# Performance work log

Measured on AMD Instinct MI355X. Metric: run time of the kernel, lower is better.

## Reference

```python
import jax, jax.numpy as jnp
import numpy as np

B, N, D = 8, 65536, 3
K = 64                 # num_centers
NPOINT = 4096
M = NPOINT // K * 2    # max_neighbors = 128
S = NPOINT // K        # fps samples per group = 64
NITER = 10             # KMeans default Niter


def _sqdist(src, dst):
    # ||s||^2 + ||d||^2 - 2 s.d   (same math as (s-d)^2 sum, GEMM form)
    s2 = (src ** 2).sum(-1)[:, :, None]          # [B,N,1]
    d2 = (dst ** 2).sum(-1)[:, None, :]          # [B,1,K]
    return s2 + d2 - 2.0 * jnp.einsum('bnd,bkd->bnk', src, dst)


def _kmeans(x):
    Bb, Nn, Dd = x.shape
    c = x[:, :K, :]
    bidx = jnp.arange(Bb)[:, None]               # broadcast with cl [B,N]
    for _ in range(NITER):
        cl = jnp.argmin(_sqdist(x, c), axis=2)   # [B,N] cluster codes
        c = jnp.zeros((Bb, K, Dd), x.dtype).at[bidx, cl].add(x)
        ncl = jnp.zeros((Bb, K), x.dtype).at[bidx, cl].add(1.0)
        c = c / ncl[:, :, None]
    return c


def _query_neighbor(x, centers):
    dist = _sqdist(x, centers)                   # [B,N,K]
    negd = -jnp.transpose(dist, (0, 2, 1))       # [B,K,N]
    _, nidx = jax.lax.top_k(negd, M)             # M nearest points per center
    bidx = jnp.arange(x.shape[0])[:, None, None]
    return x[bidx, nidx]                         # [B,K,M,3]


def _batch_fps(xyz, farthest0):
    # xyz: [B,G,Nn,3]; sequential farthest-point sampling per group
    Bb, G, Nn, _ = xyz.shape
    dist0 = jnp.full((Bb, G, Nn), 1e10, xyz.dtype)

    def step(carry, _):
        distance, farthest = carry
        centroid = jnp.take_along_axis(xyz, farthest[:, :, None, None], axis=2)  # [B,G,1,3]
        d = ((xyz - centroid) ** 2).sum(-1)       # [B,G,Nn]
        distance = jnp.minimum(distance, d)
        new_far = jnp.argmax(distance, -1).astype(farthest.dtype)
        return (distance, new_far), farthest      # store index BEFORE update

    _, idx = jax.lax.scan(step, (dist0, farthest0), None, length=S)
    idx = jnp.transpose(idx, (1, 2, 0))           # [B,G,S]
    idx3 = jnp.broadcast_to(idx[..., None], idx.shape + (3,))
    new_xyz = jnp.take_along_axis(xyz, idx3, axis=2)  # [B,G,S,3]
    return new_xyz.reshape(Bb, G * S, 3)


def setup_inputs() -> dict:
    key = jax.random.key(0)
    k1, k2 = jax.random.split(key)
    x = jax.random.normal(k1, (B, N, D), dtype=jnp.float32)
    farthest0 = jax.random.randint(k2, (B, K), 0, M, dtype=jnp.int32)
    return {"x": x, "farthest0": farthest0}


def reference(x, farthest0):
    centers = _kmeans(x)                  # [B,K,3]
    neighbor = _query_neighbor(x, centers)  # [B,K,M,3]
    new_xyz = _batch_fps(neighbor, farthest0)  # [B, NPOINT, 3]
    return new_xyz, centers
```

## Files before the change

kernel.cpp:

```cpp
#include <hip/hip_runtime.h>
#include <stdint.h>

#pragma clang fp contract(off)

#define B 8
#define N 65536
#define KC 64
#define M 128
#define S 64
#define NITER 10
#define NWAVES 16
#define HPAD 257
#define SAMPLE 8192
#define SCAP 2048
#define CAPG 3072
#define TCAP 4096
#define CSTRIDE 32
#define UPD_T 1024
#define RANGE 16384
#define NRANGE (N / RANGE)
#define PPT (RANGE / UPD_T)
#define GBATCH 2048

using u32 = unsigned int;
using u64 = unsigned long long;

__device__ __forceinline__ float sq3(float a, float b, float c) {
  return __fadd_rn(__fadd_rn(__fmul_rn(a, a), __fmul_rn(b, b)), __fmul_rn(c, c));
}
__device__ __forceinline__ float dot3(float x0, float x1, float x2,
                                      float c0, float c1, float c2) {
  return __fadd_rn(__fadd_rn(__fmul_rn(x0, c0), __fmul_rn(x1, c1)), __fmul_rn(x2, c2));
}
__device__ __forceinline__ float distf(float s2, float d2, float dt) {
  return __fsub_rn(__fadd_rn(s2, d2), __fmul_rn(2.0f, dt));
}
__device__ __forceinline__ u32 fkey(float f) {
  u32 u = __float_as_uint(f);
  return (u & 0x80000000u) ? ~u : (u | 0x80000000u);
}


__global__ void k_init_centers(const float* __restrict__ x, float* __restrict__ centers) {
  int i = blockIdx.x * blockDim.x + threadIdx.x;
  if (i >= B * KC * 3) return;
  int b = i / (KC * 3);
  int r = i % (KC * 3);
  centers[i] = x[(size_t)b * N * 3 + r];
}

__global__ void k_assign(const float* __restrict__ x, const float* __restrict__ centers,
                         unsigned char* __restrict__ cl) {
  __shared__ float4 cs[KC];
  int g = blockIdx.x;
  int b = g & 7;
  int chunk = g >> 3;
  int t = threadIdx.x;
  if (t < KC) {
    float a0 = centers[(b * KC + t) * 3 + 0];
    float a1 = centers[(b * KC + t) * 3 + 1];
    float a2 = centers[(b * KC + t) * 3 + 2];
    cs[t] = make_float4(a0, a1, a2, sq3(a0, a1, a2));
  }
  __syncthreads();
  int pr = chunk * 256 + t;
  const float2* xb2 = (const float2*)(x + (size_t)b * N * 3);
  float2 A = xb2[3 * pr], Bv = xb2[3 * pr + 1], C = xb2[3 * pr + 2];
  float s20 = sq3(A.x, A.y, Bv.x);
  float s21 = sq3(Bv.y, C.x, C.y);
  float best0 = __int_as_float(0x7f800000), best1 = best0;
  int bi0 = 0, bi1 = 0;
  for (int k = 0; k < KC; ++k) {
    float4 cc = cs[k];
    float d0 = distf(s20, cc.w, dot3(A.x, A.y, Bv.x, cc.x, cc.y, cc.z));
    float d1 = distf(s21, cc.w, dot3(Bv.y, C.x, C.y, cc.x, cc.y, cc.z));
    if (d0 < best0) { best0 = d0; bi0 = k; }
    if (d1 < best1) { best1 = d1; bi1 = k; }
  }
  *(unsigned short*)(cl + (size_t)b * N + 2 * pr) =
      (unsigned short)(bi0 | (bi1 << 8));
}

__global__ __launch_bounds__(UPD_T)
void k_cluster_update(const float* __restrict__ x, const unsigned char* __restrict__ cl,
                      float* __restrict__ centers) {
  __shared__ unsigned short midx[RANGE];
  __shared__ float bcoord[3][GBATCH + 1];
  __shared__ int woff[NWAVES];
  __shared__ int sCnt;
  int g = blockIdx.x;
  int bk = ((g & 7) << 6) | (g >> 3);
  int b = bk >> 6, k = bk & 63;
  int t = threadIdx.x, lane = t & 63, wid = t >> 6;
  const unsigned char* clb = cl + (size_t)b * N;
  const float* xb = x + (size_t)b * N * 3;
  float acc = 0.f;
  int cntAll = 0;

  for (int r = 0; r < NRANGE; ++r) {
    const uint4* cp = (const uint4*)(clb + r * RANGE);
    uint4 v = cp[t];
    u32 wsv[4] = {v.x, v.y, v.z, v.w};
    int m = 0;
#pragma unroll
    for (int j = 0; j < PPT; ++j)
      m += (((wsv[j >> 2] >> ((j & 3) * 8)) & 255u) == (u32)k);
    int incl = m;
#pragma unroll
    for (int o = 1; o < 64; o <<= 1) {
      int u = __shfl_up(incl, o);
      if (lane >= o) incl += u;
    }
    if (lane == 63) woff[wid] = incl;
    __syncthreads();
    if (t == 0) {
      int run = 0;
      for (int w = 0; w < NWAVES; ++w) { int vv = woff[w]; woff[w] = run; run += vv; }
      sCnt = run;
    }
    __syncthreads();
    int off = woff[wid] + incl - m;
    int mcnt = sCnt;
    int base = t * PPT;
#pragma unroll
    for (int j = 0; j < PPT; ++j) {
      if (((wsv[j >> 2] >> ((j & 3) * 8)) & 255u) == (u32)k)
        midx[off++] = (unsigned short)(base + j);
    }
    __syncthreads();
    for (int bo = 0; bo < mcnt; bo += GBATCH) {
      int bn = min(GBATCH, mcnt - bo);
      for (int i = t; i < bn; i += UPD_T) {
        int li = midx[bo + i];
        size_t src = ((size_t)(r * RANGE + li)) * 3;
        bcoord[0][i] = xb[src];
        bcoord[1][i] = xb[src + 1];
        bcoord[2][i] = xb[src + 2];
      }
      __syncthreads();
      if (wid == 0 && lane < 3) {
        const float* mb = &bcoord[lane][0];
        for (int i = 0; i < bn; ++i) acc = __fadd_rn(acc, mb[i]);
      }
      __syncthreads();
    }
    cntAll += mcnt;
    __syncthreads();
  }
  if (wid == 0 && lane < 3)
    centers[bk * 3 + lane] = __fdiv_rn(acc, (float)cntAll);
}

__global__ __launch_bounds__(256)
void k_thresh(const float* __restrict__ x, const float* __restrict__ centers,
              u32* __restrict__ thr, u32* __restrict__ cnt) {
  __shared__ u32 whist[4 * HPAD];
  __shared__ int sv[256];
  __shared__ u32 skeys[SCAP];
  __shared__ float4 scen;
  __shared__ u32 sSel;
  __shared__ int sNeed, sCntBin, sNum;
  int g = blockIdx.x;
  int bk = ((g & 7) << 6) | (g >> 3);
  int b = bk >> 6;
  int t = threadIdx.x, wid = t >> 6;
  if (t == 0) {
    float c0 = centers[bk * 3], c1 = centers[bk * 3 + 1], c2 = centers[bk * 3 + 2];
    scen = make_float4(c0, c1, c2, sq3(c0, c1, c2));
    cnt[bk * CSTRIDE] = 0;
    sNum = 0;
  }
  for (int i = t; i < 4 * HPAD; i += 256) whist[i] = 0;
  __syncthreads();
  float c0 = scen.x, c1 = scen.y, c2 = scen.z, d2 = scen.w;
  const float2* xb2 = (const float2*)(x + (size_t)b * N * 3);

  for (int p = t; p < SAMPLE / 2; p += 256) {
    float2 A = xb2[3 * p], Bv = xb2[3 * p + 1], C = xb2[3 * p + 2];
    float d0 = distf(sq3(A.x, A.y, Bv.x), d2, dot3(A.x, A.y, Bv.x, c0, c1, c2));
    float d1 = distf(sq3(Bv.y, C.x, C.y), d2, dot3(Bv.y, C.x, C.y, c0, c1, c2));
    atomicAdd(&whist[wid * HPAD + (fkey(d0) >> 24)], 1u);
    atomicAdd(&whist[wid * HPAD + (fkey(d1) >> 24)], 1u);
  }
  __syncthreads();
  int own = (int)(whist[0 * HPAD + t] + whist[1 * HPAD + t] +
                  whist[2 * HPAD + t] + whist[3 * HPAD + t]);
  sv[t] = own;
  __syncthreads();
  for (int off = 1; off < 256; off <<= 1) {
    int add = (t >= off) ? sv[t - off] : 0;
    __syncthreads();
    sv[t] += add;
    __syncthreads();
  }
  if (sv[t] >= M && sv[t] - own < M) {
    sSel = (u32)t; sNeed = M - (sv[t] - own); sCntBin = own;
  }
  __syncthreads();
  u32 selByte = sSel;
  int need = sNeed;
  int cntBin = sCntBin;
  u32 prefix = selByte << 24;

  if (cntBin <= SCAP) {
    for (int p = t; p < SAMPLE / 2; p += 256) {
      float2 A = xb2[3 * p], Bv = xb2[3 * p + 1], C = xb2[3 * p + 2];
      float d0 = distf(sq3(A.x, A.y, Bv.x), d2, dot3(A.x, A.y, Bv.x, c0, c1, c2));
      float d1 = distf(sq3(Bv.y, C.x, C.y), d2, dot3(Bv.y, C.x, C.y, c0, c1, c2));
      u32 k0 = fkey(d0), k1 = fkey(d1);
      if ((k0 >> 24) == selByte) skeys[atomicAdd(&sNum, 1)] = k0;
      if ((k1 >> 24) == selByte) skeys[atomicAdd(&sNum, 1)] = k1;
    }
    __syncthreads();
    int ne = sNum;
    for (int sh = 16; sh >= 0; sh -= 8) {
      whist[t] = 0;
      __syncthreads();
      for (int i = t; i < ne; i += 256) {
        u32 kk = skeys[i];
        if ((kk >> (sh + 8)) == (prefix >> (sh + 8)))
          atomicAdd(&whist[(kk >> sh) & 255u], 1u);
      }
      __syncthreads();
      int own2 = (int)whist[t];
      sv[t] = own2;
      __syncthreads();
      for (int off = 1; off < 256; off <<= 1) {
        int add = (t >= off) ? sv[t - off] : 0;
        __syncthreads();
        sv[t] += add;
        __syncthreads();
      }
      if (sv[t] >= need && sv[t] - own2 < need) {
        sSel = prefix | ((u32)t << sh);
        sNeed = need - (sv[t] - own2);
      }
      __syncthreads();
      prefix = sSel; need = sNeed;
      __syncthreads();
    }
    if (t == 0) thr[bk] = prefix;
  } else {
    if (t == 0) thr[bk] = prefix | 0x00FFFFFFu;
  }
}

__global__ __launch_bounds__(256)
void k_scatter_test(const float* __restrict__ x, const float* __restrict__ centers,
                    const u32* __restrict__ thr, u32* __restrict__ cnt,
                    u32* __restrict__ cand) {
  __shared__ float4 cs[KC];
  __shared__ u32 lthr[KC];
  __shared__ u64 wm0[4][KC], wm1[4][KC];
  __shared__ u32 wbase[4][KC];
  int g = blockIdx.x;
  int b = g & 7;
  int chunk = g >> 3;
  int t = threadIdx.x, lane = t & 63, wid = t >> 6;
  if (t < KC) {
    float a0 = centers[(b * KC + t) * 3 + 0];
    float a1 = centers[(b * KC + t) * 3 + 1];
    float a2 = centers[(b * KC + t) * 3 + 2];
    cs[t] = make_float4(a0, a1, a2, sq3(a0, a1, a2));
    lthr[t] = thr[b * KC + t];
  }
  __syncthreads();
  int pr = chunk * 256 + t;
  const float2* xb2 = (const float2*)(x + (size_t)b * N * 3);
  float2 A = xb2[3 * pr], Bv = xb2[3 * pr + 1], C = xb2[3 * pr + 2];
  float s20 = sq3(A.x, A.y, Bv.x);
  float s21 = sq3(Bv.y, C.x, C.y);
  u32 n0 = 2 * pr, n1 = 2 * pr + 1;
  u64 ltm = ((u64)1 << lane) - 1;

  for (int k = 0; k < KC; ++k) {
    float4 cc = cs[k];
    float d0 = distf(s20, cc.w, dot3(A.x, A.y, Bv.x, cc.x, cc.y, cc.z));
    float d1 = distf(s21, cc.w, dot3(Bv.y, C.x, C.y, cc.x, cc.y, cc.z));
    u64 m0 = __ballot(fkey(d0) <= lthr[k]);
    u64 m1 = __ballot(fkey(d1) <= lthr[k]);
    if (lane == 0) { wm0[wid][k] = m0; wm1[wid][k] = m1; }
  }
  __syncthreads();
  if (t < KC) {
    u32 pc[4];
    u32 total = 0;
#pragma unroll
    for (int w = 0; w < 4; ++w) {
      pc[w] = (u32)(__popcll(wm0[w][t]) + __popcll(wm1[w][t]));
      total += pc[w];
    }
    u32 base = (total > 0) ? atomicAdd(&cnt[(b * KC + t) * CSTRIDE], total) : 0u;
#pragma unroll
    for (int w = 0; w < 4; ++w) { wbase[w][t] = base; base += pc[w]; }
  }
  __syncthreads();
  u64 mybit = (u64)1 << lane;
  for (int k = 0; k < KC; ++k) {
    u64 m0 = wm0[wid][k], m1 = wm1[wid][k];
    if ((m0 | m1) == 0) continue;
    u32 wb = wbase[wid][k];
    u32* cb = cand + (size_t)(b * KC + k) * CAPG;
    if (m0 & mybit) {
      u32 pos = wb + (u32)__popcll(m0 & ltm);
      if (pos < CAPG) cb[pos] = n0;
    }
    if (m1 & mybit) {
      u32 pos = wb + (u32)__popcll(m0) + (u32)__popcll(m1 & ltm);
      if (pos < CAPG) cb[pos] = n1;
    }
  }
}

__global__ __launch_bounds__(1024)
void k_topk_sort(const float* __restrict__ x, const float* __restrict__ centers,
                 const u32* __restrict__ cnt, const u32* __restrict__ cand,
                 float* __restrict__ neighbor) {
  __shared__ u64 candList[TCAP];
  __shared__ u32 hist[256];
  __shared__ u64 lessList[M];
  __shared__ u32 eqList[256];
  __shared__ u32 sPrefix;
  __shared__ int sNeed;
  __shared__ int cntLess, cntEq;
  __shared__ float4 scen;
  int g = blockIdx.x;
  int bk = ((g & 7) << 6) | (g >> 3);
  int b = bk >> 6;
  int t = threadIdx.x;
  if (t == 0) {
    float c0 = centers[bk * 3], c1 = centers[bk * 3 + 1], c2 = centers[bk * 3 + 2];
    scen = make_float4(c0, c1, c2, sq3(c0, c1, c2));
    cntLess = 0; cntEq = 0;
  }
  __syncthreads();
  float c0 = scen.x, c1 = scen.y, c2 = scen.z, d2 = scen.w;
  const float* xb = x + (size_t)b * N * 3;
  int cc = (int)cnt[bk * CSTRIDE];

  if (cc <= CAPG) {
    const u32* cb = cand + (size_t)bk * CAPG;
    int P = M; while (P < cc) P <<= 1;
    for (int i = t; i < P; i += 1024) {
      if (i < cc) {
        u32 n = cb[i];
        float x0 = xb[n * 3], x1 = xb[n * 3 + 1], x2 = xb[n * 3 + 2];
        float d = distf(sq3(x0, x1, x2), d2, dot3(x0, x1, x2, c0, c1, c2));
        candList[i] = ((u64)fkey(d) << 32) | n;
      } else {
        candList[i] = ~0ull;
      }
    }
    __syncthreads();
    for (int ksz = 2; ksz <= P; ksz <<= 1) {
      for (int j = ksz >> 1; j > 0; j >>= 1) {
        for (int idx = t; idx < P; idx += 1024) {
          int ixj = idx ^ j;
          if (ixj > idx) {
            u64 a = candList[idx], bb = candList[ixj];
            bool up = ((idx & ksz) == 0);
            if (up ? (a > bb) : (a < bb)) { candList[idx] = bb; candList[ixj] = a; }
          }
        }
        __syncthreads();
      }
    }
    if (t < M) {
      int idx = (int)(candList[t] & 0xFFFFFFFFu);
      size_t src = ((size_t)b * N + idx) * 3;
      size_t dst = ((size_t)bk * M + t) * 3;
      neighbor[dst]     = x[src];
      neighbor[dst + 1] = x[src + 1];
      neighbor[dst + 2] = x[src + 2];
    }
    return;
  }

  u32 prefix = 0;
  int need = M;
  for (int r = 3; r >= 0; --r) {
    for (int i = t; i < 256; i += 1024) hist[i] = 0;
    __syncthreads();
    int sh = r * 8;
    for (int n = t; n < N; n += 1024) {
      float x0 = xb[n * 3], x1 = xb[n * 3 + 1], x2 = xb[n * 3 + 2];
      float d = distf(sq3(x0, x1, x2), d2, dot3(x0, x1, x2, c0, c1, c2));
      u32 key = fkey(d);
      bool ok = (r == 3) || ((key >> (sh + 8)) == (prefix >> (sh + 8)));
      if (ok) atomicAdd(&hist[(key >> sh) & 255u], 1u);
    }
    __syncthreads();
    if (t == 0) {
      int cum = 0;
      for (int bin = 0; bin < 256; ++bin) {
        int c = (int)hist[bin];
        if (cum + c >= need) { sPrefix = prefix | ((u32)bin << sh); sNeed = need - cum; break; }
        cum += c;
      }
    }
    __syncthreads();
    prefix = sPrefix; need = sNeed;
    __syncthreads();
  }
  u32 K128 = prefix;

  if (t == 0) { cntLess = 0; cntEq = 0; }
  __syncthreads();
  for (int n = t; n < N; n += 1024) {
    float x0 = xb[n * 3], x1 = xb[n * 3 + 1], x2 = xb[n * 3 + 2];
    float d = distf(sq3(x0, x1, x2), d2, dot3(x0, x1, x2, c0, c1, c2));
    u32 key = fkey(d);
    if (key < K128) {
      int p = atomicAdd(&cntLess, 1);
      if (p < M) lessList[p] = ((u64)key << 32) | (u32)n;
    } else if (key == K128) {
      int p = atomicAdd(&cntEq, 1);
      if (p < 256) eqList[p] = (u32)n;
    }
  }
  __syncthreads();
  int nl = cntLess;
  int ne2 = cntEq;
  for (int i = t; i < M; i += 1024) if (i >= nl) lessList[i] = ~0ull;
  for (int i = t; i < 256; i += 1024) if (i >= ne2) eqList[i] = 0xFFFFFFFFu;
  __syncthreads();

  for (int ksz = 2; ksz <= M; ksz <<= 1) {
    for (int j = ksz >> 1; j > 0; j >>= 1) {
      for (int idx = t; idx < M; idx += 1024) {
        int ixj = idx ^ j;
        if (ixj > idx) {
          u64 a = lessList[idx], bb = lessList[ixj];
          bool up = ((idx & ksz) == 0);
          if (up ? (a > bb) : (a < bb)) { lessList[idx] = bb; lessList[ixj] = a; }
        }
      }
      __syncthreads();
    }
  }
  for (int ksz = 2; ksz <= 256; ksz <<= 1) {
    for (int j = ksz >> 1; j > 0; j >>= 1) {
      for (int idx = t; idx < 256; idx += 1024) {
        int ixj = idx ^ j;
        if (ixj > idx) {
          u32 a = eqList[idx], bb = eqList[ixj];
          bool up = ((idx & ksz) == 0);
          if (up ? (a > bb) : (a < bb)) { eqList[idx] = bb; eqList[ixj] = a; }
        }
      }
      __syncthreads();
    }
  }

  if (t < M) {
    int idx = (t < nl) ? (int)(lessList[t] & 0xFFFFFFFFu) : (int)eqList[t - nl];
    size_t src = ((size_t)b * N + idx) * 3;
    size_t dst = ((size_t)bk * M + t) * 3;
    neighbor[dst]     = x[src];
    neighbor[dst + 1] = x[src + 1];
    neighbor[dst + 2] = x[src + 2];
  }
}

__global__ void k_fps(const float* __restrict__ neighbor, const int* __restrict__ farthest0,
                      const float* __restrict__ centers, float* __restrict__ out) {
  __shared__ float px[M], py[M], pz[M];
  __shared__ float wv[2];
  __shared__ int wi[2];
  int bg = blockIdx.x;
  int b = bg >> 6, g = bg & 63;
  int t = threadIdx.x;
  {
    int i = bg * 128 + t;
    if (i < B * KC * 3) out[B * 4096 * 3 + i] = centers[i];
  }
  size_t src = ((size_t)bg * M + t) * 3;
  float mx = neighbor[src], my = neighbor[src + 1], mz = neighbor[src + 2];
  px[t] = mx; py[t] = my; pz[t] = mz;
  int far = farthest0[bg];
  float dist = 1e10f;
  __syncthreads();
  for (int s = 0; s < S; ++s) {
    if (t == far) {
      size_t dst = ((size_t)b * 4096 + g * 64 + s) * 3;
      out[dst] = mx; out[dst + 1] = my; out[dst + 2] = mz;
    }
    float cx = px[far], cy = py[far], cz = pz[far];
    float dx = __fsub_rn(mx, cx), dy = __fsub_rn(my, cy), dz = __fsub_rn(mz, cz);
    float d = sq3(dx, dy, dz);
    dist = fminf(dist, d);
    float v = dist;
    int i = t;
#pragma unroll
    for (int off = 1; off < 64; off <<= 1) {
      float ov = __shfl_xor(v, off);
      int oi = __shfl_xor(i, off);
      if (ov > v || (ov == v && oi < i)) { v = ov; i = oi; }
    }
    int wid = t >> 6;
    if ((t & 63) == 0) { wv[wid] = v; wi[wid] = i; }
    __syncthreads();
    float v0 = wv[0]; int i0 = wi[0];
    float v1 = wv[1]; int i1 = wi[1];
    far = (v1 > v0 || (v1 == v0 && i1 < i0)) ? i1 : i0;
    __syncthreads();
  }
}

extern "C" void kernel_launch(void* const* d_in, const int* in_sizes, int n_in,
                              void* d_out, int out_size, void* d_ws, size_t ws_size,
                              hipStream_t stream) {
  const float* x = (const float*)d_in[0];
  const int* farthest0 = (const int*)d_in[1];
  float* out = (float*)d_out;

  char* w = (char*)d_ws;
  float* centers         = (float*)(w);
  unsigned char* cl      = (unsigned char*)(w + 8192);
  u32* thr               = (u32*)(w + 8192 + 524288);
  u32* cnt               = (u32*)(w + 8192 + 524288 + 4096);
  float* neighbor        = (float*)(w + 8192 + 524288 + 4096 + 65536);
  u32* cand              = (u32*)(w + 8192 + 524288 + 4096 + 65536 + 786432);

  k_init_centers<<<6, 256, 0, stream>>>(x, centers);
  for (int it = 0; it < NITER; ++it) {
    k_assign<<<B * 128, 256, 0, stream>>>(x, centers, cl);
    k_cluster_update<<<B * KC, UPD_T, 0, stream>>>(x, cl, centers);
  }
  k_thresh<<<B * KC, 256, 0, stream>>>(x, centers, thr, cnt);
  k_scatter_test<<<B * 128, 256, 0, stream>>>(x, centers, thr, cnt, cand);
  k_topk_sort<<<B * KC, 1024, 0, stream>>>(x, centers, cnt, cand, neighbor);
  k_fps<<<B * KC, M, 0, stream>>>(neighbor, farthest0, centers, out);
}
```

Measured before the change: 513.9 us.

## Replace candidate bitonic sort with radix select, widen assign to four points per thread

The top-k kernel no longer bitonic-sorts every candidate, up to 3072 of them. It runs a 4-pass radix select over the candidate keys, using a wave-level prefix scan to locate the threshold bin. It then compacts the survivors into a 512-slot buffer, sorts only that buffer, and falls back to the full-N path if more than 512 keys survive. The block size drops to 256 threads. Separately, k_assign now handles four points per thread using float4 loads, on half as many blocks, and the cluster-update summation loop is unrolled.

```diff
diff --git a/kernel.cpp b/kernel.cpp
--- a/kernel.cpp
+++ b/kernel.cpp
@@ -14,7 +14,7 @@
 #define SAMPLE 8192
 #define SCAP 2048
 #define CAPG 3072
-#define TCAP 4096
+#define WCAP 512
 #define CSTRIDE 32
 #define UPD_T 1024
 #define RANGE 16384
@@ -49,8 +49,9 @@
   centers[i] = x[(size_t)b * N * 3 + r];
 }
 
-__global__ void k_assign(const float* __restrict__ x, const float* __restrict__ centers,
-                         unsigned char* __restrict__ cl) {
+__global__ __launch_bounds__(256)
+void k_assign(const float* __restrict__ x, const float* __restrict__ centers,
+              unsigned char* __restrict__ cl) {
   __shared__ float4 cs[KC];
   int g = blockIdx.x;
   int b = g & 7;
@@ -63,22 +64,33 @@
     cs[t] = make_float4(a0, a1, a2, sq3(a0, a1, a2));
   }
   __syncthreads();
-  int pr = chunk * 256 + t;
-  const float2* xb2 = (const float2*)(x + (size_t)b * N * 3);
-  float2 A = xb2[3 * pr], Bv = xb2[3 * pr + 1], C = xb2[3 * pr + 2];
-  float s20 = sq3(A.x, A.y, Bv.x);
-  float s21 = sq3(Bv.y, C.x, C.y);
-  float best0 = __int_as_float(0x7f800000), best1 = best0;
-  int bi0 = 0, bi1 = 0;
+  int q = chunk * 256 + t;
+  const float4* xb4 = (const float4*)(x + (size_t)b * N * 3);
+  float4 A = xb4[3 * q], Bv = xb4[3 * q + 1], C = xb4[3 * q + 2];
+  float p0x = A.x, p0y = A.y, p0z = A.z;
+  float p1x = A.w, p1y = Bv.x, p1z = Bv.y;
+  float p2x = Bv.z, p2y = Bv.w, p2z = C.x;
+  float p3x = C.y, p3y = C.z, p3z = C.w;
+  float s0 = sq3(p0x, p0y, p0z);
+  float s1 = sq3(p1x, p1y, p1z);
+  float s2 = sq3(p2x, p2y, p2z);
+  float s3 = sq3(p3x, p3y, p3z);
+  float inf = __int_as_float(0x7f800000);
+  float b0 = inf, b1 = inf, b2 = inf, b3 = inf;
+  int i0 = 0, i1 = 0, i2 = 0, i3 = 0;
   for (int k = 0; k < KC; ++k) {
     float4 cc = cs[k];
-    float d0 = distf(s20, cc.w, dot3(A.x, A.y, Bv.x, cc.x, cc.y, cc.z));
-    float d1 = distf(s21, cc.w, dot3(Bv.y, C.x, C.y, cc.x, cc.y, cc.z));
-    if (d0 < best0) { best0 = d0; bi0 = k; }
-    if (d1 < best1) { best1 = d1; bi1 = k; }
-  }
-  *(unsigned short*)(cl + (size_t)b * N + 2 * pr) =
-      (unsigned short)(bi0 | (bi1 << 8));
+    float d0 = distf(s0, cc.w, dot3(p0x, p0y, p0z, cc.x, cc.y, cc.z));
+    float d1 = distf(s1, cc.w, dot3(p1x, p1y, p1z, cc.x, cc.y, cc.z));
+    float d2 = distf(s2, cc.w, dot3(p2x, p2y, p2z, cc.x, cc.y, cc.z));
+    float d3 = distf(s3, cc.w, dot3(p3x, p3y, p3z, cc.x, cc.y, cc.z));
+    if (d0 < b0) { b0 = d0; i0 = k; }
+    if (d1 < b1) { b1 = d1; i1 = k; }
+    if (d2 < b2) { b2 = d2; i2 = k; }
+    if (d3 < b3) { b3 = d3; i3 = k; }
+  }
+  *(u32*)(cl + (size_t)b * N + 4 * q) =
+      (u32)i0 | ((u32)i1 << 8) | ((u32)i2 << 16) | ((u32)i3 << 24);
 }
 
 __global__ __launch_bounds__(UPD_T)
@@ -140,6 +152,7 @@
       __syncthreads();
       if (wid == 0 && lane < 3) {
         const float* mb = &bcoord[lane][0];
+#pragma unroll 8
         for (int i = 0; i < bn; ++i) acc = __fadd_rn(acc, mb[i]);
       }
       __syncthreads();
@@ -312,26 +325,27 @@
   }
 }
 
-__global__ __launch_bounds__(1024)
+__global__ __launch_bounds__(256)
 void k_topk_sort(const float* __restrict__ x, const float* __restrict__ centers,
                  const u32* __restrict__ cnt, const u32* __restrict__ cand,
                  float* __restrict__ neighbor) {
-  __shared__ u64 candList[TCAP];
+  __shared__ u64 candList[CAPG];
   __shared__ u32 hist[256];
+  __shared__ u64 wbuf[WCAP];
   __shared__ u64 lessList[M];
   __shared__ u32 eqList[256];
-  __shared__ u32 sPrefix;
+  __shared__ u32 sSel;
   __shared__ int sNeed;
-  __shared__ int cntLess, cntEq;
+  __shared__ int cntW, cntLess, cntEq;
   __shared__ float4 scen;
   int g = blockIdx.x;
   int bk = ((g & 7) << 6) | (g >> 3);
   int b = bk >> 6;
-  int t = threadIdx.x;
+  int t = threadIdx.x, lane = t & 63, wid = t >> 6;
   if (t == 0) {
     float c0 = centers[bk * 3], c1 = centers[bk * 3 + 1], c2 = centers[bk * 3 + 2];
     scen = make_float4(c0, c1, c2, sq3(c0, c1, c2));
-    cntLess = 0; cntEq = 0;
+    cntW = 0;
   }
   __syncthreads();
   float c0 = scen.x, c1 = scen.y, c2 = scen.z, d2 = scen.w;
@@ -340,49 +354,99 @@
 
   if (cc <= CAPG) {
     const u32* cb = cand + (size_t)bk * CAPG;
-    int P = M; while (P < cc) P <<= 1;
-    for (int i = t; i < P; i += 1024) {
-      if (i < cc) {
-        u32 n = cb[i];
-        float x0 = xb[n * 3], x1 = xb[n * 3 + 1], x2 = xb[n * 3 + 2];
-        float d = distf(sq3(x0, x1, x2), d2, dot3(x0, x1, x2, c0, c1, c2));
-        candList[i] = ((u64)fkey(d) << 32) | n;
-      } else {
-        candList[i] = ~0ull;
-      }
-    }
-    __syncthreads();
-    for (int ksz = 2; ksz <= P; ksz <<= 1) {
-      for (int j = ksz >> 1; j > 0; j >>= 1) {
-        for (int idx = t; idx < P; idx += 1024) {
-          int ixj = idx ^ j;
-          if (ixj > idx) {
-            u64 a = candList[idx], bb = candList[ixj];
-            bool up = ((idx & ksz) == 0);
-            if (up ? (a > bb) : (a < bb)) { candList[idx] = bb; candList[ixj] = a; }
+    for (int i = t; i < cc; i += 256) {
+      u32 n = cb[i];
+      float x0 = xb[n * 3], x1 = xb[n * 3 + 1], x2 = xb[n * 3 + 2];
+      float d = distf(sq3(x0, x1, x2), d2, dot3(x0, x1, x2, c0, c1, c2));
+      candList[i] = ((u64)fkey(d) << 32) | n;
+    }
+    __syncthreads();
+    u32 prefix = 0;
+    int need = M;
+    for (int r = 3; r >= 0; --r) {
+      int sh = r * 8;
+      hist[t] = 0;
+      __syncthreads();
+      for (int i = t; i < cc; i += 256) {
+        u32 key = (u32)(candList[i] >> 32);
+        bool ok = (r == 3) || ((key >> (sh + 8)) == (prefix >> (sh + 8)));
+        if (ok) atomicAdd(&hist[(key >> sh) & 255u], 1u);
+      }
+      __syncthreads();
+      if (wid == 0) {
+        u32 h0 = hist[4 * lane + 0], h1 = hist[4 * lane + 1];
+        u32 h2 = hist[4 * lane + 2], h3 = hist[4 * lane + 3];
+        u32 lsum = h0 + h1 + h2 + h3;
+        u32 incl = lsum;
+#pragma unroll
+        for (int o = 1; o < 64; o <<= 1) {
+          u32 u = __shfl_up(incl, o);
+          if (lane >= o) incl += u;
+        }
+        u32 excl = incl - lsum;
+        if ((int)excl < need && need <= (int)incl) {
+          u32 hh[4] = {h0, h1, h2, h3};
+          u32 cum = excl; int bin = -1; u32 bc = 0;
+#pragma unroll
+          for (int j = 0; j < 4; ++j) {
+            if (bin < 0 && (int)(cum + hh[j]) >= need) { bin = 4 * lane + j; bc = cum; }
+            cum += hh[j];
           }
+          sSel = prefix | ((u32)bin << sh);
+          sNeed = need - (int)bc;
         }
-        __syncthreads();
-      }
-    }
-    if (t < M) {
-      int idx = (int)(candList[t] & 0xFFFFFFFFu);
-      size_t src = ((size_t)b * N + idx) * 3;
-      size_t dst = ((size_t)bk * M + t) * 3;
-      neighbor[dst]     = x[src];
-      neighbor[dst + 1] = x[src + 1];
-      neighbor[dst + 2] = x[src + 2];
-    }
-    return;
-  }
-
+      }
+      __syncthreads();
+      prefix = sSel; need = sNeed;
+      __syncthreads();
+    }
+    u32 K128 = prefix;
+    for (int i = t; i < cc; i += 256) {
+      u64 e = candList[i];
+      if ((u32)(e >> 32) <= K128) {
+        int p = atomicAdd(&cntW, 1);
+        if (p < WCAP) wbuf[p] = e;
+      }
+    }
+    __syncthreads();
+    int wcnt = cntW;
+    if (wcnt <= WCAP) {
+      for (int i = t; i < WCAP; i += 256) if (i >= wcnt) wbuf[i] = ~0ull;
+      __syncthreads();
+      for (int ksz = 2; ksz <= WCAP; ksz <<= 1) {
+        for (int j = ksz >> 1; j > 0; j >>= 1) {
+          for (int idx = t; idx < WCAP; idx += 256) {
+            int ixj = idx ^ j;
+            if (ixj > idx) {
+              u64 a = wbuf[idx], bb = wbuf[ixj];
+              bool up = ((idx & ksz) == 0);
+              if (up ? (a > bb) : (a < bb)) { wbuf[idx] = bb; wbuf[ixj] = a; }
+            }
+          }
+          __syncthreads();
+        }
+      }
+      if (t < M) {
+        int idx = (int)(wbuf[t] & 0xFFFFFFFFu);
+        size_t src = ((size_t)b * N + idx) * 3;
+        size_t dst = ((size_t)bk * M + t) * 3;
+        neighbor[dst]     = x[src];
+        neighbor[dst + 1] = x[src + 1];
+        neighbor[dst + 2] = x[src + 2];
+      }
+      return;
+    }
+  }
+
+  if (t == 0) { cntLess = 0; cntEq = 0; }
+  __syncthreads();
   u32 prefix = 0;
   int need = M;
   for (int r = 3; r >= 0; --r) {
-    for (int i = t; i < 256; i += 1024) hist[i] = 0;
+    for (int i = t; i < 256; i += 256) hist[i] = 0;
     __syncthreads();
     int sh = r * 8;
-    for (int n = t; n < N; n += 1024) {
+    for (int n = t; n < N; n += 256) {
       float x0 = xb[n * 3], x1 = xb[n * 3 + 1], x2 = xb[n * 3 + 2];
       float d = distf(sq3(x0, x1, x2), d2, dot3(x0, x1, x2, c0, c1, c2));
       u32 key = fkey(d);
@@ -394,19 +458,17 @@
       int cum = 0;
       for (int bin = 0; bin < 256; ++bin) {
         int c = (int)hist[bin];
-        if (cum + c >= need) { sPrefix = prefix | ((u32)bin << sh); sNeed = need - cum; break; }
+        if (cum + c >= need) { sSel = prefix | ((u32)bin << sh); sNeed = need - cum; break; }
         cum += c;
       }
     }
     __syncthreads();
-    prefix = sPrefix; need = sNeed;
+    prefix = sSel; need = sNeed;
     __syncthreads();
   }
   u32 K128 = prefix;
 
-  if (t == 0) { cntLess = 0; cntEq = 0; }
-  __syncthreads();
-  for (int n = t; n < N; n += 1024) {
+  for (int n = t; n < N; n += 256) {
     float x0 = xb[n * 3], x1 = xb[n * 3 + 1], x2 = xb[n * 3 + 2];
     float d = distf(sq3(x0, x1, x2), d2, dot3(x0, x1, x2, c0, c1, c2));
     u32 key = fkey(d);
@@ -421,13 +483,13 @@
   __syncthreads();
   int nl = cntLess;
   int ne2 = cntEq;
-  for (int i = t; i < M; i += 1024) if (i >= nl) lessList[i] = ~0ull;
-  for (int i = t; i < 256; i += 1024) if (i >= ne2) eqList[i] = 0xFFFFFFFFu;
+  for (int i = t; i < M; i += 256) if (i >= nl) lessList[i] = ~0ull;
+  for (int i = t; i < 256; i += 256) if (i >= ne2) eqList[i] = 0xFFFFFFFFu;
   __syncthreads();
 
   for (int ksz = 2; ksz <= M; ksz <<= 1) {
     for (int j = ksz >> 1; j > 0; j >>= 1) {
-      for (int idx = t; idx < M; idx += 1024) {
+      for (int idx = t; idx < M; idx += 256) {
         int ixj = idx ^ j;
         if (ixj > idx) {
           u64 a = lessList[idx], bb = lessList[ixj];
@@ -440,7 +502,7 @@
   }
   for (int ksz = 2; ksz <= 256; ksz <<= 1) {
     for (int j = ksz >> 1; j > 0; j >>= 1) {
-      for (int idx = t; idx < 256; idx += 1024) {
+      for (int idx = t; idx < 256; idx += 256) {
         int ixj = idx ^ j;
         if (ixj > idx) {
           u32 a = eqList[idx], bb = eqList[ixj];
@@ -524,11 +586,11 @@
 
   k_init_centers<<<6, 256, 0, stream>>>(x, centers);
   for (int it = 0; it < NITER; ++it) {
-    k_assign<<<B * 128, 256, 0, stream>>>(x, centers, cl);
+    k_assign<<<B * 64, 256, 0, stream>>>(x, centers, cl);
     k_cluster_update<<<B * KC, UPD_T, 0, stream>>>(x, cl, centers);
   }
   k_thresh<<<B * KC, 256, 0, stream>>>(x, centers, thr, cnt);
   k_scatter_test<<<B * 128, 256, 0, stream>>>(x, centers, thr, cnt, cand);
-  k_topk_sort<<<B * KC, 1024, 0, stream>>>(x, centers, cnt, cand, neighbor);
+  k_topk_sort<<<B * KC, 256, 0, stream>>>(x, centers, cnt, cand, neighbor);
   k_fps<<<B * KC, M, 0, stream>>>(neighbor, farthest0, centers, out);
 }
```

After: 500.4 us. 1.03x faster.
